# Performance work log

Hardware: AMD Instinct MI355X
Metric: run time of the kernel (lower is better)

The kernel has to match this reference:

```python
import jax, jax.numpy as jnp
import numpy as np

B, T, D, H = 4, 2048, 2048, 16
HD = D // H

def setup_inputs() -> dict:
    key = jax.random.key(0)
    k1, k2, k3 = jax.random.split(key, 3)
    x = jax.random.normal(k1, (B, T, D), dtype=jnp.float32)
    mask = jnp.ones((B, T), dtype=jnp.int32)
    # torch Linear weights, scaled like default init (~1/sqrt(fan_in))
    w_qkv = jax.random.normal(k2, (3 * D, D), dtype=jnp.float32) / np.sqrt(D)
    w_o = jax.random.normal(k3, (D, D), dtype=jnp.float32) / np.sqrt(D)
    return {"x": x, "mask": mask, "w_qkv": w_qkv, "w_o": w_o}

def reference(x, mask, w_qkv, w_o):
    # qkv projection: (B,T,D) @ (D,3D) -> (B,T,3D)
    qkv = jnp.einsum('btd,ed->bte', x, w_qkv)
    q, k, v = jnp.split(qkv, 3, axis=-1)
    # (B,T,D) -> (B,H,T,HD)
    def to_heads(t):
        return t.reshape(B, T, H, HD).transpose(0, 2, 1, 3)
    q, k, v = to_heads(q), to_heads(k), to_heads(v)
    scale = 1.0 / np.sqrt(HD).astype(np.float32)
    att = jnp.einsum('bhqd,bhkd->bhqk', q, k) * scale  # (B,H,T,T)
    att = jnp.where(mask[:, None, None, :] == 0, -jnp.inf, att)
    att = jax.nn.softmax(att, axis=-1)
    y = jnp.einsum('bhqk,bhkd->bhqd', att, v)  # (B,H,T,HD)
    y = y.transpose(0, 2, 1, 3).reshape(B, T, D)
    return jnp.einsum('btd,ed->bte', y, w_o)
```

## Files before the change

kernel.cpp:

```cpp
#include <hip/hip_runtime.h>
#include <hip/hip_bf16.h>

typedef __bf16 bf16;
typedef bf16 bf16x8 __attribute__((ext_vector_type(8)));
typedef float f32x4 __attribute__((ext_vector_type(4)));

struct alignas(8) bh4 { bf16 v[4]; };

__device__ __forceinline__ void glds16(const bf16* g, bf16* l) {
  __builtin_amdgcn_global_load_lds(
      (const __attribute__((address_space(1))) void*)g,
      (__attribute__((address_space(3))) void*)l, 16, 0, 0);
}

#define QSCALE (1.4426950408889634f / 11.313708498984761f)

__global__ void convert_to_bf16(const float* __restrict__ s, bf16* __restrict__ dst,
                                long n) {
  const long stride = (long)gridDim.x * blockDim.x * 8;
  for (long i = ((long)blockIdx.x * blockDim.x + threadIdx.x) * 8; i < n; i += stride) {
    float4 a = *(const float4*)(s + i);
    float4 b = *(const float4*)(s + i + 4);
    bf16x8 o;
    o[0] = (bf16)a.x; o[1] = (bf16)a.y; o[2] = (bf16)a.z; o[3] = (bf16)a.w;
    o[4] = (bf16)b.x; o[5] = (bf16)b.y; o[6] = (bf16)b.z; o[7] = (bf16)b.w;
    *(bf16x8*)(dst + i) = o;
  }
}

template <int MODE>
__global__ void gemm_bt(const bf16* __restrict__ A, const bf16* __restrict__ Bw,
                        void* __restrict__ C0v, bf16* __restrict__ C1,
                        bf16* __restrict__ C2, int M, int N, int K) {
  __shared__ __align__(16) bf16 sA[128 * 32];
  __shared__ __align__(16) bf16 sB[128 * 32];
  const int tid = threadIdx.x;
  const int lane = tid & 63, wid = tid >> 6;
  const int wm = wid & 1, wn = wid >> 1;
  const int quad = lane >> 4, l16 = lane & 15;
  const int bm = blockIdx.y * 128, bn = blockIdx.x * 128;

  f32x4 acc[4][4] = {};

  const int srow = tid >> 2, scol = (tid & 3) << 3;
  const bf16* gA = A + (size_t)(bm + srow) * K + scol;
  const bf16* gB = Bw + (size_t)(bn + srow) * K + scol;
  const size_t row64 = (size_t)64 * K;

  for (int k0 = 0; k0 < K; k0 += 32) {
    glds16(gA + k0, &sA[tid * 8]);
    glds16(gA + k0 + row64, &sA[2048 + tid * 8]);
    glds16(gB + k0, &sB[tid * 8]);
    glds16(gB + k0 + row64, &sB[2048 + tid * 8]);
    __syncthreads();
    bf16x8 af[4], bff[4];
#pragma unroll
    for (int mt = 0; mt < 4; ++mt)
      af[mt] = *(const bf16x8*)&sA[(wm * 64 + mt * 16 + l16) * 32 + quad * 8];
#pragma unroll
    for (int nt = 0; nt < 4; ++nt)
      bff[nt] = *(const bf16x8*)&sB[(wn * 64 + nt * 16 + l16) * 32 + quad * 8];
#pragma unroll
    for (int mt = 0; mt < 4; ++mt)
#pragma unroll
      for (int nt = 0; nt < 4; ++nt)
        acc[mt][nt] = __builtin_amdgcn_mfma_f32_16x16x32_bf16(af[mt], bff[nt], acc[mt][nt], 0, 0, 0);
    __syncthreads();
  }

  if (MODE == 0) {
    bf16* C0 = (bf16*)C0v;
    const int which = blockIdx.x >> 4;
    const int h = blockIdx.x & 15;
#pragma unroll
    for (int mt = 0; mt < 4; ++mt) {
      const int m0 = bm + wm * 64 + mt * 16 + quad * 4;
      const int b = m0 >> 11, t0 = m0 & 2047;
#pragma unroll
      for (int nt = 0; nt < 4; ++nt) {
        const int hd = wn * 64 + nt * 16 + l16;
        if (which == 0) {
          bf16* dst = C0 + (((size_t)(b * 16 + h) * 2048 + t0) * 128 + hd);
#pragma unroll
          for (int r = 0; r < 4; ++r) dst[(size_t)r * 128] = (bf16)(acc[mt][nt][r] * QSCALE);
        } else if (which == 1) {
          bf16* dst = C1 + (((size_t)(b * 16 + h) * 2048 + t0) * 128 + hd);
#pragma unroll
          for (int r = 0; r < 4; ++r) dst[(size_t)r * 128] = (bf16)acc[mt][nt][r];
        } else {
          bh4 pk;
#pragma unroll
          for (int r = 0; r < 4; ++r) pk.v[r] = (bf16)acc[mt][nt][r];
          *(bh4*)(C2 + ((size_t)((b * 16 + h) * 128 + hd) * 2048 + t0)) = pk;
        }
      }
    }
  } else {
    float* C0 = (float*)C0v;
#pragma unroll
    for (int mt = 0; mt < 4; ++mt) {
      const int m0 = bm + wm * 64 + mt * 16 + quad * 4;
#pragma unroll
      for (int nt = 0; nt < 4; ++nt) {
        const int n = bn + wn * 64 + nt * 16 + l16;
#pragma unroll
        for (int r = 0; r < 4; ++r)
          C0[(size_t)(m0 + r) * N + n] = acc[mt][nt][r];
      }
    }
  }
}

__global__ __launch_bounds__(256, 3)
void attn_kernel(const bf16* __restrict__ Q, const bf16* __restrict__ Kb,
                 const bf16* __restrict__ Vt, const int* __restrict__ mask,
                 bf16* __restrict__ Y) {
  __shared__ __align__(16) bf16 smem[25600];
  bf16* sK = smem;
  bf16* sV = smem + 8192;
  bf16* sP = smem + 16384;

  const int tid = threadIdx.x;
  const int lane = tid & 63, w = tid >> 6;
  const int quad = lane >> 4, l16 = lane & 15;
  const int bh = blockIdx.x, b = bh >> 4, h = bh & 15;
  const int qt = blockIdx.y;
  const size_t head = (size_t)bh * (2048 * 128);

  bf16x8 qf[2][4];
#pragma unroll
  for (int nt = 0; nt < 2; ++nt) {
    const int t = qt * 128 + w * 32 + nt * 16 + l16;
    const bf16* g = Q + head + (size_t)t * 128 + quad * 8;
#pragma unroll
    for (int kk = 0; kk < 4; ++kk)
      qf[nt][kk] = *(const bf16x8*)(g + kk * 32);
  }

  f32x4 o[8][2] = {};
  float mrow[2] = {-3.0e38f, -3.0e38f};
  float lrow[2] = {0.0f, 0.0f};

  const int* maskb = mask + b * 2048;
  bf16* sPw = sP + w * (32 * 72);

  for (int kt = 0; kt < 32; ++kt) {
    const int key0 = kt * 64;
    {
      const int cp = lane & 15;
      const int rbase = w * 16 + (lane >> 4);
#pragma unroll
      for (int p = 0; p < 4; ++p) {
        const int row = rbase + p * 4;
        const int c = (cp & 8) | ((cp ^ row) & 7);
        glds16(Kb + head + (size_t)(key0 + row) * 128 + c * 8,
               &sK[(w * 16 + p * 4) * 128 + lane * 8]);
      }
    }
    {
      const int cp = lane & 7;
      const int rbase = w * 32 + (lane >> 3);
#pragma unroll
      for (int p = 0; p < 4; ++p) {
        const int row = rbase + p * 8;
        const int c = cp ^ (row & 7);
        glds16(Vt + head + (size_t)row * 2048 + key0 + c * 8,
               &sV[(w * 32 + p * 8) * 64 + lane * 8]);
      }
    }
    __syncthreads();

    f32x4 st[4][2] = {};
#pragma unroll
    for (int kk = 0; kk < 4; ++kk) {
      bf16x8 ak[4];
#pragma unroll
      for (int mt = 0; mt < 4; ++mt) {
        const int row = mt * 16 + l16;
        const int c = kk * 4 + quad;
        const int cp = (c & 8) | ((c ^ row) & 7);
        ak[mt] = *(const bf16x8*)&sK[row * 128 + cp * 8];
      }
#pragma unroll
      for (int mt = 0; mt < 4; ++mt)
#pragma unroll
        for (int nt = 0; nt < 2; ++nt)
          st[mt][nt] = __builtin_amdgcn_mfma_f32_16x16x32_bf16(ak[mt], qf[nt][kk], st[mt][nt], 0, 0, 0);
    }

    const int4* mp = (const int4*)(maskb + key0);
    int4 mm[4];
#pragma unroll
    for (int mt = 0; mt < 4; ++mt) mm[mt] = mp[mt * 4 + quad];

#pragma unroll
    for (int nt = 0; nt < 2; ++nt) {
      float mx = -1.0e30f;
#pragma unroll
      for (int mt = 0; mt < 4; ++mt) {
        const int* mi = (const int*)&mm[mt];
#pragma unroll
        for (int r = 0; r < 4; ++r) {
          float v = (mi[r] != 0) ? st[mt][nt][r] : -1.0e30f;
          st[mt][nt][r] = v;
          mx = fmaxf(mx, v);
        }
      }
      mx = fmaxf(mx, __shfl_xor(mx, 16));
      mx = fmaxf(mx, __shfl_xor(mx, 32));
      const float newm = fmaxf(mrow[nt], mx);
      const float alpha = exp2f(mrow[nt] - newm);
      mrow[nt] = newm;
      float rs = 0.0f;
#pragma unroll
      for (int mt = 0; mt < 4; ++mt) {
        const int* mi = (const int*)&mm[mt];
        bh4 pk;
#pragma unroll
        for (int r = 0; r < 4; ++r) {
          const float p = (mi[r] != 0) ? exp2f(st[mt][nt][r] - newm) : 0.0f;
          rs += p;
          pk.v[r] = (bf16)p;
        }
        *(bh4*)&sPw[(nt * 16 + l16) * 72 + mt * 16 + quad * 4] = pk;
      }
      rs += __shfl_xor(rs, 16);
      rs += __shfl_xor(rs, 32);
      lrow[nt] = lrow[nt] * alpha + rs;
#pragma unroll
      for (int mt = 0; mt < 8; ++mt)
#pragma unroll
        for (int r = 0; r < 4; ++r)
          o[mt][nt][r] *= alpha;
    }

#pragma unroll
    for (int kk = 0; kk < 2; ++kk) {
      bf16x8 bp[2];
#pragma unroll
      for (int nt = 0; nt < 2; ++nt)
        bp[nt] = *(const bf16x8*)&sPw[(nt * 16 + l16) * 72 + kk * 32 + quad * 8];
#pragma unroll
      for (int mt = 0; mt < 8; ++mt) {
        const int row = mt * 16 + l16;
        const int c = kk * 4 + quad;
        bf16x8 av = *(const bf16x8*)&sV[row * 64 + (c ^ (row & 7)) * 8];
#pragma unroll
        for (int nt = 0; nt < 2; ++nt)
          o[mt][nt] = __builtin_amdgcn_mfma_f32_16x16x32_bf16(av, bp[nt], o[mt][nt], 0, 0, 0);
      }
    }
    __syncthreads();
  }

  bf16* sOw = smem + w * 4352;
#pragma unroll
  for (int nt = 0; nt < 2; ++nt) {
    const float inv = 1.0f / lrow[nt];
#pragma unroll
    for (int mt = 0; mt < 8; ++mt) {
      bh4 pk;
#pragma unroll
      for (int r = 0; r < 4; ++r) pk.v[r] = (bf16)(o[mt][nt][r] * inv);
      *(bh4*)&sOw[(nt * 16 + l16) * 136 + mt * 16 + quad * 4] = pk;
    }
  }
  {
    const int col = (lane & 15) * 8;
#pragma unroll
    for (int p = 0; p < 8; ++p) {
      const int row = p * 4 + (lane >> 4);
      int4 v = *(const int4*)&sOw[row * 136 + col];
      const int token = qt * 128 + w * 32 + row;
      *(int4*)(Y + ((size_t)(b * 2048 + token)) * 2048 + h * 128 + col) = v;
    }
  }
}

extern "C" void kernel_launch(void* const* d_in, const int* in_sizes, int n_in,
                              void* d_out, int out_size, void* d_ws, size_t ws_size,
                              hipStream_t stream) {
  const float* x_raw  = (const float*)d_in[0];
  const int*   mask   = (const int*)d_in[1];
  const float* wq_raw = (const float*)d_in[2];
  const float* wo_raw = (const float*)d_in[3];
  float* out = (float*)d_out;

  char* ws = (char*)d_ws;
  const size_t MB = 1024 * 1024;
  bf16* xb  = (bf16*)(ws + 256);
  bf16* wqb = (bf16*)(ws + 256 + 32 * MB);
  bf16* qb  = (bf16*)(ws + 256 + 56 * MB);
  bf16* kb  = (bf16*)(ws + 256 + 88 * MB);
  bf16* vt  = (bf16*)(ws + 256 + 120 * MB);
  bf16* yb  = xb;
  bf16* wob = wqb;

  convert_to_bf16<<<1024, 256, 0, stream>>>(x_raw, xb, (long)in_sizes[0]);
  convert_to_bf16<<<1024, 256, 0, stream>>>(wq_raw, wqb, (long)in_sizes[2]);

  gemm_bt<0><<<dim3(48, 64), 256, 0, stream>>>(xb, wqb, qb, kb, vt, 8192, 6144, 2048);

  convert_to_bf16<<<1024, 256, 0, stream>>>(wo_raw, wob, (long)in_sizes[3]);

  attn_kernel<<<dim3(64, 16), 256, 0, stream>>>(qb, kb, vt, mask, yb);

  gemm_bt<1><<<dim3(16, 64), 256, 0, stream>>>(yb, wob, out, nullptr, nullptr, 8192, 2048, 2048);
}
```

Baseline: 748.8 us.

## Prefetch K via registers, skip mask work for full tiles, defer softmax rescale

```diff
diff --git a/kernel.cpp b/kernel.cpp
--- a/kernel.cpp
+++ b/kernel.cpp
@@ -14,6 +14,7 @@
 }
 
 #define QSCALE (1.4426950408889634f / 11.313708498984761f)
+#define DEFER_THR 8.0f
 
 __global__ void convert_to_bf16(const float* __restrict__ s, bf16* __restrict__ dst,
                                 long n) {
@@ -144,31 +145,52 @@
   const int* maskb = mask + b * 2048;
   bf16* sPw = sP + w * (32 * 72);
 
+  unsigned long long vmask;
+  {
+    const int4* mp4 = (const int4*)maskb;
+    bool ok = true;
+#pragma unroll
+    for (int j = 0; j < 8; ++j) {
+      const int4 q4 = mp4[lane * 8 + j];
+      ok = ok && (q4.x != 0) && (q4.y != 0) && (q4.z != 0) && (q4.w != 0);
+    }
+    vmask = __ballot(ok);
+  }
+
+  const int cpK = lane & 15, rbK = w * 16 + (lane >> 4);
+  const int cpV = lane & 7,  rbV = w * 32 + (lane >> 3);
+
+  int4 kreg[4];
+  auto ldk = [&](int kt2) {
+    const int key0 = kt2 * 64;
+#pragma unroll
+    for (int p = 0; p < 4; ++p) {
+      const int row = rbK + p * 4;
+      const int c = (cpK & 8) | ((cpK ^ row) & 7);
+      kreg[p] = *(const int4*)(Kb + head + (size_t)(key0 + row) * 128 + c * 8);
+    }
+  };
+
+  ldk(0);
+
   for (int kt = 0; kt < 32; ++kt) {
     const int key0 = kt * 64;
-    {
-      const int cp = lane & 15;
-      const int rbase = w * 16 + (lane >> 4);
-#pragma unroll
-      for (int p = 0; p < 4; ++p) {
-        const int row = rbase + p * 4;
-        const int c = (cp & 8) | ((cp ^ row) & 7);
-        glds16(Kb + head + (size_t)(key0 + row) * 128 + c * 8,
-               &sK[(w * 16 + p * 4) * 128 + lane * 8]);
-      }
-    }
-    {
-      const int cp = lane & 7;
-      const int rbase = w * 32 + (lane >> 3);
-#pragma unroll
-      for (int p = 0; p < 4; ++p) {
-        const int row = rbase + p * 8;
-        const int c = cp ^ (row & 7);
-        glds16(Vt + head + (size_t)row * 2048 + key0 + c * 8,
-               &sV[(w * 32 + p * 8) * 64 + lane * 8]);
-      }
-    }
     __syncthreads();
+
+#pragma unroll
+    for (int p = 0; p < 4; ++p) {
+      const int row = rbV + p * 8;
+      const int c = cpV ^ (row & 7);
+      glds16(Vt + head + (size_t)row * 2048 + key0 + c * 8,
+             &sV[(w * 32 + p * 8) * 64 + lane * 8]);
+    }
+#pragma unroll
+    for (int p = 0; p < 4; ++p)
+      *(int4*)&sK[(rbK + p * 4) * 128 + cpK * 8] = kreg[p];
+
+    __syncthreads();
+
+    if (kt < 31) ldk(kt + 1);
 
     f32x4 st[4][2] = {};
 #pragma unroll
@@ -188,50 +210,90 @@
           st[mt][nt] = __builtin_amdgcn_mfma_f32_16x16x32_bf16(ak[mt], qf[nt][kk], st[mt][nt], 0, 0, 0);
     }
 
-    const int4* mp = (const int4*)(maskb + key0);
-    int4 mm[4];
-#pragma unroll
-    for (int mt = 0; mt < 4; ++mt) mm[mt] = mp[mt * 4 + quad];
-
-#pragma unroll
-    for (int nt = 0; nt < 2; ++nt) {
-      float mx = -1.0e30f;
-#pragma unroll
-      for (int mt = 0; mt < 4; ++mt) {
-        const int* mi = (const int*)&mm[mt];
-#pragma unroll
-        for (int r = 0; r < 4; ++r) {
-          float v = (mi[r] != 0) ? st[mt][nt][r] : -1.0e30f;
-          st[mt][nt][r] = v;
-          mx = fmaxf(mx, v);
-        }
-      }
-      mx = fmaxf(mx, __shfl_xor(mx, 16));
-      mx = fmaxf(mx, __shfl_xor(mx, 32));
-      const float newm = fmaxf(mrow[nt], mx);
-      const float alpha = exp2f(mrow[nt] - newm);
-      mrow[nt] = newm;
-      float rs = 0.0f;
-#pragma unroll
-      for (int mt = 0; mt < 4; ++mt) {
-        const int* mi = (const int*)&mm[mt];
-        bh4 pk;
-#pragma unroll
-        for (int r = 0; r < 4; ++r) {
-          const float p = (mi[r] != 0) ? exp2f(st[mt][nt][r] - newm) : 0.0f;
-          rs += p;
-          pk.v[r] = (bf16)p;
-        }
-        *(bh4*)&sPw[(nt * 16 + l16) * 72 + mt * 16 + quad * 4] = pk;
-      }
-      rs += __shfl_xor(rs, 16);
-      rs += __shfl_xor(rs, 32);
-      lrow[nt] = lrow[nt] * alpha + rs;
-#pragma unroll
-      for (int mt = 0; mt < 8; ++mt)
-#pragma unroll
-        for (int r = 0; r < 4; ++r)
-          o[mt][nt][r] *= alpha;
+    const bool tileok = ((vmask >> (2 * kt)) & 3ULL) == 3ULL;
+
+    if (tileok) {
+#pragma unroll
+      for (int nt = 0; nt < 2; ++nt) {
+        float mx = -1.0e30f;
+#pragma unroll
+        for (int mt = 0; mt < 4; ++mt)
+#pragma unroll
+          for (int r = 0; r < 4; ++r) mx = fmaxf(mx, st[mt][nt][r]);
+        mx = fmaxf(mx, __shfl_xor(mx, 16));
+        mx = fmaxf(mx, __shfl_xor(mx, 32));
+        if (!__all(mx <= mrow[nt] + DEFER_THR)) {
+          const float newm = fmaxf(mrow[nt], mx);
+          const float alpha = exp2f(mrow[nt] - newm);
+          mrow[nt] = newm;
+          lrow[nt] *= alpha;
+#pragma unroll
+          for (int mt = 0; mt < 8; ++mt)
+#pragma unroll
+            for (int r = 0; r < 4; ++r) o[mt][nt][r] *= alpha;
+        }
+        const float m = mrow[nt];
+        float rs = 0.0f;
+#pragma unroll
+        for (int mt = 0; mt < 4; ++mt) {
+          bh4 pk;
+#pragma unroll
+          for (int r = 0; r < 4; ++r) {
+            const float p = exp2f(st[mt][nt][r] - m);
+            rs += p;
+            pk.v[r] = (bf16)p;
+          }
+          *(bh4*)&sPw[(nt * 16 + l16) * 72 + mt * 16 + quad * 4] = pk;
+        }
+        rs += __shfl_xor(rs, 16);
+        rs += __shfl_xor(rs, 32);
+        lrow[nt] += rs;
+      }
+    } else {
+      const int4* mp = (const int4*)(maskb + key0);
+      int4 mm[4];
+#pragma unroll
+      for (int mt = 0; mt < 4; ++mt) mm[mt] = mp[mt * 4 + quad];
+#pragma unroll
+      for (int nt = 0; nt < 2; ++nt) {
+        float mx = -1.0e30f;
+#pragma unroll
+        for (int mt = 0; mt < 4; ++mt) {
+          const int* mi = (const int*)&mm[mt];
+#pragma unroll
+          for (int r = 0; r < 4; ++r) {
+            float v = (mi[r] != 0) ? st[mt][nt][r] : -1.0e30f;
+            st[mt][nt][r] = v;
+            mx = fmaxf(mx, v);
+          }
+        }
+        mx = fmaxf(mx, __shfl_xor(mx, 16));
+        mx = fmaxf(mx, __shfl_xor(mx, 32));
+        const float newm = fmaxf(mrow[nt], mx);
+        const float alpha = exp2f(mrow[nt] - newm);
+        mrow[nt] = newm;
+        float rs = 0.0f;
+#pragma unroll
+        for (int mt = 0; mt < 4; ++mt) {
+          const int* mi = (const int*)&mm[mt];
+          bh4 pk;
+#pragma unroll
+          for (int r = 0; r < 4; ++r) {
+            const float p = (mi[r] != 0) ? exp2f(st[mt][nt][r] - newm) : 0.0f;
+            rs += p;
+            pk.v[r] = (bf16)p;
+          }
+          *(bh4*)&sPw[(nt * 16 + l16) * 72 + mt * 16 + quad * 4] = pk;
+        }
+        rs += __shfl_xor(rs, 16);
+        rs += __shfl_xor(rs, 32);
+        lrow[nt] = lrow[nt] * alpha + rs;
+#pragma unroll
+        for (int mt = 0; mt < 8; ++mt)
+#pragma unroll
+          for (int r = 0; r < 4; ++r)
+            o[mt][nt][r] *= alpha;
+      }
     }
 
 #pragma unroll
@@ -250,8 +312,9 @@
           o[mt][nt] = __builtin_amdgcn_mfma_f32_16x16x32_bf16(av, bp[nt], o[mt][nt], 0, 0, 0);
       }
     }
-    __syncthreads();
-  }
+  }
+
+  __syncthreads();
 
   bf16* sOw = smem + w * 4352;
 #pragma unroll
```

Result: slower. 1.185 ms (+58.3%).
